# Kernel tuning notes

Hardware: AMD Instinct MI355X
Metric: run time of the kernel (lower is better)

The kernel has to match this reference:

```python
import jax, jax.numpy as jnp
import numpy as np

D = 768
EPS = 1e-5

def _layernorm(x, g, b):
    mu = jnp.mean(x, axis=-1, keepdims=True)
    var = jnp.mean(jnp.square(x - mu), axis=-1, keepdims=True)
    return (x - mu) * jax.lax.rsqrt(var + EPS) * g + b

def setup_inputs() -> dict:
    key = jax.random.key(0)
    ks = jax.random.split(key, 12)
    s = 1.0 / np.sqrt(D)
    x = jax.random.normal(ks[0], (8, 2048, D), dtype=jnp.float32)
    Wq = jax.random.uniform(ks[1], (D, D), jnp.float32, -s, s)
    bq = jax.random.uniform(ks[2], (D,), jnp.float32, -s, s)
    Wk = jax.random.uniform(ks[3], (D, D), jnp.float32, -s, s)
    bk = jax.random.uniform(ks[4], (D,), jnp.float32, -s, s)
    Wv = jax.random.uniform(ks[5], (D, D), jnp.float32, -s, s)
    bv = jax.random.uniform(ks[6], (D,), jnp.float32, -s, s)
    W1 = jax.random.uniform(ks[7], (D, D), jnp.float32, -s, s)
    b1 = jax.random.uniform(ks[8], (D,), jnp.float32, -s, s)
    W2 = jax.random.uniform(ks[9], (D, D), jnp.float32, -s, s)
    b2 = jax.random.uniform(ks[10], (D,), jnp.float32, -s, s)
    g_n1 = jnp.ones((D,), jnp.float32); be_n1 = jnp.zeros((D,), jnp.float32)
    g_n2 = jnp.ones((D,), jnp.float32); be_n2 = jnp.zeros((D,), jnp.float32)
    return {"x": x, "Wq": Wq, "bq": bq, "Wk": Wk, "bk": bk, "Wv": Wv, "bv": bv,
            "W1": W1, "b1": b1, "W2": W2, "b2": b2,
            "g_n1": g_n1, "be_n1": be_n1, "g_n2": g_n2, "be_n2": be_n2}

def reference(x, Wq, bq, Wk, bk, Wv, bv, W1, b1, W2, b2, g_n1, be_n1, g_n2, be_n2):
    # pre-norm single-head self-attention (scores materialized as in source)
    h = _layernorm(x, g_n1, be_n1)
    q = h @ Wq.T + bq  # [B,S,D]
    k = h @ Wk.T + bk
    v = h @ Wv.T + bv
    scores = jnp.einsum('bsd,btd->bst', q, k) / jnp.sqrt(jnp.float32(D))
    attn = jax.nn.softmax(scores, axis=-1)
    x = jnp.einsum('bst,btd->bsd', attn, v) + x
    # MLP: two Linear(d,d) each followed by exact GELU (matches source MLP)
    h = _layernorm(x, g_n2, be_n2)
    h = jax.nn.gelu(h @ W1.T + b1, approximate=False)
    h = jax.nn.gelu(h @ W2.T + b2, approximate=False)
    return h + x
```

## Files before the change

kernel.cpp:

```cpp
#include <hip/hip_runtime.h>
#include <cstdint>
#include <cstddef>

#define D_MODEL 768
#define NBATCH 8
#define SEQLEN 2048
#define NROWS (NBATCH*SEQLEN)

typedef __attribute__((ext_vector_type(4))) float  f32x4;
typedef __attribute__((ext_vector_type(8))) __bf16 bf16x8;
typedef __attribute__((ext_vector_type(4))) __bf16 bf16x4;
typedef __attribute__((ext_vector_type(8))) _Float16 f16x8;

#define MFMA16(a,b,c) __builtin_amdgcn_mfma_f32_16x16x32_bf16(a,b,c,0,0,0)
#define SCALE 0.03608439182435161f
#define AS1 __attribute__((address_space(1)))
#define AS3 __attribute__((address_space(3)))

static constexpr size_t SZ_ACT = (size_t)NROWS * D_MODEL * 2;
static constexpr size_t OFF_Q    = 0;
static constexpr size_t OFF_K    = OFF_Q + SZ_ACT;
static constexpr size_t OFF_VT   = OFF_K + SZ_ACT;
static constexpr size_t OFF_X2   = OFF_VT + SZ_ACT;
static constexpr size_t OFF_W    = OFF_X2 + (size_t)NROWS*D_MODEL*4;
static constexpr size_t OFF_POOL = OFF_W + (size_t)5*589824*2;

__device__ __forceinline__ float gelu_exact(float x) {
  return 0.5f * x * (1.0f + erff(x * 0.70710678118654752f));
}

__device__ __forceinline__ int xcd_remap(int p, int chunk) {
  return (p & 7) * chunk + (p >> 3);
}

__global__ __launch_bounds__(256) void k_cvt5(
    const float* __restrict__ s0, const float* __restrict__ s1,
    const float* __restrict__ s2, const float* __restrict__ s3,
    const float* __restrict__ s4, __bf16* __restrict__ dst)
{
  const int wsel = blockIdx.y;
  const float* s = wsel==0 ? s0 : wsel==1 ? s1 : wsel==2 ? s2 : wsel==3 ? s3 : s4;
  const size_t i = ((size_t)blockIdx.x*256 + threadIdx.x)*4;
  float4 v = *(const float4*)(s + i);
  bf16x4 o;
  o[0] = (__bf16)v.x; o[1] = (__bf16)v.y; o[2] = (__bf16)v.z; o[3] = (__bf16)v.w;
  *(bf16x4*)(dst + (size_t)wsel*589824 + i) = o;
}

__global__ __launch_bounds__(256) void k_layernorm(
    const float* __restrict__ x, const float* __restrict__ g,
    const float* __restrict__ be, __bf16* __restrict__ out)
{
  const int row  = blockIdx.x*4 + (threadIdx.x>>6);
  const int lane = threadIdx.x & 63;
  const float4* xr = (const float4*)(x + (size_t)row*D_MODEL);
  float4 v[3];
  float s = 0.f, ss = 0.f;
#pragma unroll
  for (int j=0;j<3;j++){
    v[j] = xr[lane + 64*j];
    s  += v[j].x + v[j].y + v[j].z + v[j].w;
    ss += v[j].x*v[j].x + v[j].y*v[j].y + v[j].z*v[j].z + v[j].w*v[j].w;
  }
#pragma unroll
  for (int d=1; d<64; d<<=1){ s += __shfl_xor(s,d); ss += __shfl_xor(ss,d); }
  const float mu   = s  * (1.f/768.f);
  const float var  = ss * (1.f/768.f) - mu*mu;
  const float rstd = rsqrtf(var + 1e-5f);
  __bf16* orow = out + (size_t)row*D_MODEL;
#pragma unroll
  for (int j=0;j<3;j++){
    const int c0 = (lane + 64*j)*4;
    bf16x4 o;
    o[0] = (__bf16)((v[j].x - mu)*rstd*g[c0+0] + be[c0+0]);
    o[1] = (__bf16)((v[j].y - mu)*rstd*g[c0+1] + be[c0+1]);
    o[2] = (__bf16)((v[j].z - mu)*rstd*g[c0+2] + be[c0+2]);
    o[3] = (__bf16)((v[j].w - mu)*rstd*g[c0+3] + be[c0+3]);
    *(bf16x4*)(orow + c0) = o;
  }
}

__global__ __launch_bounds__(256) void k_softmax(_Float16* __restrict__ S)
{
  const int row  = blockIdx.x*4 + (threadIdx.x>>6);
  const int lane = threadIdx.x & 63;
  _Float16* sr = S + (size_t)row*SEQLEN + lane*32;
  f16x8 v[4];
#pragma unroll
  for (int j=0;j<4;j++) v[j] = *(const f16x8*)(sr + j*8);
  float f[32];
  float mx = -1e30f;
#pragma unroll
  for (int j=0;j<4;j++)
#pragma unroll
    for (int e=0;e<8;e++){ f[j*8+e] = (float)v[j][e]; mx = fmaxf(mx, f[j*8+e]); }
#pragma unroll
  for (int d=1; d<64; d<<=1) mx = fmaxf(mx, __shfl_xor(mx, d));
  float sum = 0.f;
#pragma unroll
  for (int i=0;i<32;i++){ f[i] = __expf(f[i]-mx); sum += f[i]; }
#pragma unroll
  for (int d=1; d<64; d<<=1) sum += __shfl_xor(sum, d);
  const float inv = 1.f/sum;
  __bf16* pr = (__bf16*)(S + (size_t)row*SEQLEN) + lane*32;
#pragma unroll
  for (int j=0;j<4;j++){
    bf16x8 o;
#pragma unroll
    for (int e=0;e<8;e++) o[e] = (__bf16)(f[j*8+e]*inv);
    *(bf16x8*)(pr + j*8) = o;
  }
}

template<int NT>
__device__ __forceinline__ void gemm_core_rp(
    const __bf16* __restrict__ Asrc, const int ldA,
    const __bf16* __restrict__ Bsrc, const int ldB,
    f32x4 (&acc)[4][4])
{
  __shared__ __bf16 As[2*4096];
  __shared__ __bf16 Bs[2*4096];
  const int tid = threadIdx.x, w = tid>>6, lane = tid&63;
  const int wr = w>>1, wc = w&1, l16 = lane&15, l4 = lane>>4;

  const int rql   = l16>>1;
  const int rslot = (((l16&1)<<2) + l4) ^ rql;
  const int roff  = rql*64 + rslot*8;

  const int su  = (lane&7) ^ (lane>>3);
  const int ss_ = (su>>2)&1;
  const int sg_ = su&3;
  const int srw = 2*(lane>>3) + ss_;
  const int sco = sg_*8;

#pragma unroll
  for (int mi=0;mi<4;mi++)
#pragma unroll
    for (int ni=0;ni<4;ni++)
      acc[mi][ni] = (f32x4){0.f,0.f,0.f,0.f};

#define STGRP(T_) { \
    const int kb_ = (T_)*32; \
    const int sb_ = ((T_)&1)*4096; \
    _Pragma("unroll") \
    for (int i_=0;i_<2;i_++){ \
      const int ii_ = w + i_*4; \
      const int rg_ = ii_*16 + srw; \
      __builtin_amdgcn_global_load_lds((const AS1 void*)(Asrc + (size_t)rg_*ldA + kb_ + sco), (AS3 void*)(As + sb_ + ii_*512), 16, 0, 0); \
      __builtin_amdgcn_global_load_lds((const AS1 void*)(Bsrc + (size_t)rg_*ldB + kb_ + sco), (AS3 void*)(Bs + sb_ + ii_*512), 16, 0, 0); \
    } }

  STGRP(0) STGRP(1)

  for (int t=0; t<NT; ++t){
    if (t+1 < NT) asm volatile("s_waitcnt vmcnt(4)" ::: "memory");
    else          asm volatile("s_waitcnt vmcnt(0)" ::: "memory");
    __builtin_amdgcn_s_barrier();
    const int sb = (t&1)*4096;
    bf16x8 af[4], bq[4];
#pragma unroll
    for (int mi=0;mi<4;mi++)
      af[mi] = *(const bf16x8*)(As + sb + (wr*32 + mi*8)*64 + roff);
#pragma unroll
    for (int ni=0;ni<4;ni++)
      bq[ni] = *(const bf16x8*)(Bs + sb + (wc*32 + ni*8)*64 + roff);
    asm volatile("s_waitcnt lgkmcnt(0)" ::: "memory");
    __builtin_amdgcn_sched_barrier(0);
    __builtin_amdgcn_s_barrier();
    if (t+2 < NT) STGRP(t+2)
    __builtin_amdgcn_s_setprio(1);
#pragma unroll
    for (int mi=0;mi<4;mi++)
#pragma unroll
      for (int ni=0;ni<4;ni++)
        acc[mi][ni] = MFMA16(af[mi], bq[ni], acc[mi][ni]);
    __builtin_amdgcn_s_setprio(0);
  }
#undef STGRP
}

__global__ __launch_bounds__(256) void k_qkv(
    const __bf16* __restrict__ A, const __bf16* __restrict__ W,
    const float* __restrict__ bq, const float* __restrict__ bk, const float* __restrict__ bv,
    __bf16* __restrict__ Cq, __bf16* __restrict__ Ck, __bf16* __restrict__ vT)
{
  const int L = xcd_remap(blockIdx.x, 288);
  const int bm = L/18, bn = L%18;
  f32x4 acc[4][4];
  gemm_core_rp<24>(A + (size_t)bm*128*D_MODEL, D_MODEL, W + (size_t)bn*128*D_MODEL, D_MODEL, acc);
  const int tid = threadIdx.x, w=tid>>6, lane=tid&63;
  const int wr=w>>1, wc=w&1, l16=lane&15, l4=lane>>4;
  const int seg = bn/6;
  const int colb = (bn%6)*128 + wc*64;
  const int row0 = bm*128 + wr*64;
  if (seg < 2){
    const float* bias = seg==0 ? bq : bk;
    __bf16* C = seg==0 ? Cq : Ck;
#pragma unroll
    for (int ni=0;ni<4;ni++){
      const int col = colb + ni*16 + l16;
      const float bb = bias[col];
#pragma unroll
      for (int mi=0;mi<4;mi++)
#pragma unroll
        for (int r=0;r<4;r++){
          const int row = row0 + mi*16 + l4*4 + r;
          float v = acc[mi][ni][r] + bb;
          if (seg==0) v *= SCALE;
          C[(size_t)row*D_MODEL + col] = (__bf16)v;
        }
    }
  } else {
    const int b = row0 >> 11;
    const int trow0 = row0 & 2047;
    __bf16* vtb = vT + (size_t)b*D_MODEL*SEQLEN;
#pragma unroll
    for (int ni=0;ni<4;ni++){
      const int col = colb + ni*16 + l16;
      const float bb = bv[col];
#pragma unroll
      for (int mi=0;mi<4;mi++){
        bf16x4 o;
#pragma unroll
        for (int r=0;r<4;r++) o[r] = (__bf16)(acc[mi][ni][r] + bb);
        *(bf16x4*)(vtb + (size_t)col*SEQLEN + trow0 + mi*16 + l4*4) = o;
      }
    }
  }
}

__global__ __launch_bounds__(256) void k_s(
    const __bf16* __restrict__ Q, const __bf16* __restrict__ K, _Float16* __restrict__ S,
    int chunk)
{
  const int L = xcd_remap(blockIdx.x, chunk);
  const int batch = L>>8, r = L&255;
  const int bm = r>>4, bn = r&15;
  const size_t bo = (size_t)batch * SEQLEN * D_MODEL;
  f32x4 acc[4][4];
  gemm_core_rp<24>(Q + bo + (size_t)bm*128*D_MODEL, D_MODEL, K + bo + (size_t)bn*128*D_MODEL, D_MODEL, acc);
  const int tid = threadIdx.x, w=tid>>6, lane=tid&63;
  const int wr=w>>1, wc=w&1, l16=lane&15, l4=lane>>4;
  _Float16* Sb = S + (size_t)batch*SEQLEN*SEQLEN;
  const int row0 = bm*128 + wr*64, col0 = bn*128 + wc*64;
#pragma unroll
  for (int ni=0;ni<4;ni++){
    const int col = col0 + ni*16 + l16;
#pragma unroll
    for (int mi=0;mi<4;mi++)
#pragma unroll
      for (int r2=0;r2<4;r2++)
        Sb[(size_t)(row0 + mi*16 + l4*4 + r2)*SEQLEN + col] = (_Float16)acc[mi][ni][r2];
  }
}

__global__ __launch_bounds__(256) void k_pv(
    const __bf16* __restrict__ P, const __bf16* __restrict__ VT,
    const float* __restrict__ x, float* __restrict__ x2, int bbase, int chunk)
{
  const int L = xcd_remap(blockIdx.x, chunk);
  const int by = L/96, r = L%96;
  const int bm = r/6, bn = r%6;
  const int bidx = bbase + by;
  f32x4 acc[4][4];
  gemm_core_rp<64>(P + (size_t)by*SEQLEN*SEQLEN + (size_t)bm*128*SEQLEN, SEQLEN,
                   VT + (size_t)bidx*D_MODEL*SEQLEN + (size_t)bn*128*SEQLEN, SEQLEN, acc);
  const int tid = threadIdx.x, w=tid>>6, lane=tid&63;
  const int wr=w>>1, wc=w&1, l16=lane&15, l4=lane>>4;
  const size_t row0 = (size_t)bidx*SEQLEN + bm*128 + wr*64;
  const int col0 = bn*128 + wc*64;
#pragma unroll
  for (int ni=0;ni<4;ni++){
    const int col = col0 + ni*16 + l16;
#pragma unroll
    for (int mi=0;mi<4;mi++)
#pragma unroll
      for (int r2=0;r2<4;r2++){
        const size_t row = row0 + mi*16 + l4*4 + r2;
        x2[row*D_MODEL + col] = acc[mi][ni][r2] + x[row*D_MODEL + col];
      }
  }
}

template<int RES>
__global__ __launch_bounds__(256) void k_mlp(
    const __bf16* __restrict__ A, const __bf16* __restrict__ W,
    const float* __restrict__ bias, const float* __restrict__ resid, void* __restrict__ out)
{
  const int L = xcd_remap(blockIdx.x, 96);
  const int bm = L/6, bn = L%6;
  f32x4 acc[4][4];
  gemm_core_rp<24>(A + (size_t)bm*128*D_MODEL, D_MODEL, W + (size_t)bn*128*D_MODEL, D_MODEL, acc);
  const int tid = threadIdx.x, w=tid>>6, lane=tid&63;
  const int wr=w>>1, wc=w&1, l16=lane&15, l4=lane>>4;
  const int row0 = bm*128 + wr*64, col0 = bn*128 + wc*64;
#pragma unroll
  for (int ni=0;ni<4;ni++){
    const int col = col0 + ni*16 + l16;
    const float bb = bias[col];
#pragma unroll
    for (int mi=0;mi<4;mi++)
#pragma unroll
      for (int r=0;r<4;r++){
        const int row = row0 + mi*16 + l4*4 + r;
        float v = gelu_exact(acc[mi][ni][r] + bb);
        if (RES) ((float*)out)[(size_t)row*D_MODEL + col] = v + resid[(size_t)row*D_MODEL + col];
        else     ((__bf16*)out)[(size_t)row*D_MODEL + col] = (__bf16)v;
      }
  }
}

extern "C" void kernel_launch(void* const* d_in, const int* in_sizes, int n_in,
                              void* d_out, int out_size, void* d_ws, size_t ws_size,
                              hipStream_t stream)
{
  const float* x   = (const float*)d_in[0];
  const float* Wq  = (const float*)d_in[1];
  const float* bq  = (const float*)d_in[2];
  const float* Wk  = (const float*)d_in[3];
  const float* bk  = (const float*)d_in[4];
  const float* Wv  = (const float*)d_in[5];
  const float* bv  = (const float*)d_in[6];
  const float* W1  = (const float*)d_in[7];
  const float* b1  = (const float*)d_in[8];
  const float* W2  = (const float*)d_in[9];
  const float* b2  = (const float*)d_in[10];
  const float* g1  = (const float*)d_in[11];
  const float* be1 = (const float*)d_in[12];
  const float* g2  = (const float*)d_in[13];
  const float* be2 = (const float*)d_in[14];
  (void)in_sizes; (void)n_in; (void)out_size;

  char* ws = (char*)d_ws;
  __bf16*   qb  = (__bf16*)(ws + OFF_Q);
  __bf16*   kb  = (__bf16*)(ws + OFF_K);
  __bf16*   vT  = (__bf16*)(ws + OFF_VT);
  float*    x2  = (float*)(ws + OFF_X2);
  __bf16*   wbf = (__bf16*)(ws + OFF_W);
  __bf16*   h1  = (__bf16*)(ws + OFF_POOL);
  _Float16* Sp  = (_Float16*)(ws + OFF_POOL);
  __bf16*   h2  = h1;
  __bf16*   h3  = qb;

  const bool big = ws_size >= OFF_POOL + (size_t)NBATCH*SEQLEN*SEQLEN*2;

  k_cvt5<<<dim3(576,5,1),256,0,stream>>>(Wq,Wk,Wv,W1,W2,wbf);
  k_layernorm<<<dim3(4096),256,0,stream>>>(x, g1, be1, h1);
  k_qkv<<<dim3(2304),256,0,stream>>>(h1, wbf, bq, bk, bv, qb, kb, vT);

  if (big){
    k_s<<<dim3(2048),256,0,stream>>>(qb, kb, Sp, 256);
    k_softmax<<<dim3(4096),256,0,stream>>>(Sp);
    k_pv<<<dim3(768),256,0,stream>>>((const __bf16*)Sp, vT, x, x2, 0, 96);
  } else {
    for (int c=0;c<2;c++){
      const size_t qoff = (size_t)c*4*SEQLEN*D_MODEL;
      k_s<<<dim3(1024),256,0,stream>>>(qb + qoff, kb + qoff, Sp, 128);
      k_softmax<<<dim3(2048),256,0,stream>>>(Sp);
      k_pv<<<dim3(384),256,0,stream>>>((const __bf16*)Sp, vT, x, x2, c*4, 48);
    }
  }

  k_layernorm<<<dim3(4096),256,0,stream>>>(x2, g2, be2, h2);
  k_mlp<0><<<dim3(768),256,0,stream>>>(h2, wbf + (size_t)3*589824, b1, nullptr, h3);
  k_mlp<1><<<dim3(768),256,0,stream>>>(h3, wbf + (size_t)4*589824, b2, x2, d_out);
}
```

Before: 384.7 us.

## Replace double-buffered GEMM core with single-buffer BK=64 swizzled tile loop

The shared GEMM core moves from a two-stage double-buffered pipeline with a K tile of 32 to a single-buffer loop with a K tile of 64. It now loads, waits for all loads, computes two MFMA substeps and then synchronises, so it runs half as many iterations and barriers per tile. It also uses a simpler XOR swizzle to avoid LDS bank conflicts. The cost is that global loads no longer overlap with MFMA work inside a block, so latency hiding depends on other resident blocks. LDS per block is unchanged.

```diff
diff --git a/kernel.cpp b/kernel.cpp
--- a/kernel.cpp
+++ b/kernel.cpp
@@ -113,25 +113,18 @@
 }
 
 template<int NT>
-__device__ __forceinline__ void gemm_core_rp(
+__device__ __forceinline__ void gemm_core_sb(
     const __bf16* __restrict__ Asrc, const int ldA,
     const __bf16* __restrict__ Bsrc, const int ldB,
     f32x4 (&acc)[4][4])
 {
-  __shared__ __bf16 As[2*4096];
-  __shared__ __bf16 Bs[2*4096];
+  __shared__ __bf16 As[128*64];
+  __shared__ __bf16 Bs[128*64];
   const int tid = threadIdx.x, w = tid>>6, lane = tid&63;
   const int wr = w>>1, wc = w&1, l16 = lane&15, l4 = lane>>4;
-
-  const int rql   = l16>>1;
-  const int rslot = (((l16&1)<<2) + l4) ^ rql;
-  const int roff  = rql*64 + rslot*8;
-
-  const int su  = (lane&7) ^ (lane>>3);
-  const int ss_ = (su>>2)&1;
-  const int sg_ = su&3;
-  const int srw = 2*(lane>>3) + ss_;
-  const int sco = sg_*8;
+  const int sro = lane>>3;
+  const int sgr = ((lane&7) ^ (lane>>3))*8;
+  const int rxr = l16 & 7;
 
 #pragma unroll
   for (int mi=0;mi<4;mi++)
@@ -139,44 +132,40 @@
     for (int ni=0;ni<4;ni++)
       acc[mi][ni] = (f32x4){0.f,0.f,0.f,0.f};
 
-#define STGRP(T_) { \
-    const int kb_ = (T_)*32; \
-    const int sb_ = ((T_)&1)*4096; \
-    _Pragma("unroll") \
-    for (int i_=0;i_<2;i_++){ \
-      const int ii_ = w + i_*4; \
-      const int rg_ = ii_*16 + srw; \
-      __builtin_amdgcn_global_load_lds((const AS1 void*)(Asrc + (size_t)rg_*ldA + kb_ + sco), (AS3 void*)(As + sb_ + ii_*512), 16, 0, 0); \
-      __builtin_amdgcn_global_load_lds((const AS1 void*)(Bsrc + (size_t)rg_*ldB + kb_ + sco), (AS3 void*)(Bs + sb_ + ii_*512), 16, 0, 0); \
-    } }
-
-  STGRP(0) STGRP(1)
-
   for (int t=0; t<NT; ++t){
-    if (t+1 < NT) asm volatile("s_waitcnt vmcnt(4)" ::: "memory");
-    else          asm volatile("s_waitcnt vmcnt(0)" ::: "memory");
+#pragma unroll
+    for (int i=0;i<4;i++){
+      const int strip = w*4 + i;
+      const int rg = strip*8 + sro;
+      __builtin_amdgcn_global_load_lds(
+        (const AS1 void*)(Asrc + (size_t)rg*ldA + t*64 + sgr),
+        (AS3 void*)(As + strip*512), 16, 0, 0);
+      __builtin_amdgcn_global_load_lds(
+        (const AS1 void*)(Bsrc + (size_t)rg*ldB + t*64 + sgr),
+        (AS3 void*)(Bs + strip*512), 16, 0, 0);
+    }
+    asm volatile("s_waitcnt vmcnt(0)" ::: "memory");
     __builtin_amdgcn_s_barrier();
-    const int sb = (t&1)*4096;
-    bf16x8 af[4], bq[4];
-#pragma unroll
-    for (int mi=0;mi<4;mi++)
-      af[mi] = *(const bf16x8*)(As + sb + (wr*32 + mi*8)*64 + roff);
-#pragma unroll
-    for (int ni=0;ni<4;ni++)
-      bq[ni] = *(const bf16x8*)(Bs + sb + (wc*32 + ni*8)*64 + roff);
-    asm volatile("s_waitcnt lgkmcnt(0)" ::: "memory");
-    __builtin_amdgcn_sched_barrier(0);
+
+#pragma unroll
+    for (int kk=0;kk<2;kk++){
+      bf16x8 af[4], bq[4];
+#pragma unroll
+      for (int mi=0;mi<4;mi++)
+        af[mi] = *(const bf16x8*)(As + (wr*64 + mi*16 + l16)*64 + (((kk*4 + l4) ^ rxr))*8);
+#pragma unroll
+      for (int ni=0;ni<4;ni++)
+        bq[ni] = *(const bf16x8*)(Bs + (wc*64 + ni*16 + l16)*64 + (((kk*4 + l4) ^ rxr))*8);
+      __builtin_amdgcn_s_setprio(1);
+#pragma unroll
+      for (int mi=0;mi<4;mi++)
+#pragma unroll
+        for (int ni=0;ni<4;ni++)
+          acc[mi][ni] = MFMA16(af[mi], bq[ni], acc[mi][ni]);
+      __builtin_amdgcn_s_setprio(0);
+    }
     __builtin_amdgcn_s_barrier();
-    if (t+2 < NT) STGRP(t+2)
-    __builtin_amdgcn_s_setprio(1);
-#pragma unroll
-    for (int mi=0;mi<4;mi++)
-#pragma unroll
-      for (int ni=0;ni<4;ni++)
-        acc[mi][ni] = MFMA16(af[mi], bq[ni], acc[mi][ni]);
-    __builtin_amdgcn_s_setprio(0);
-  }
-#undef STGRP
+  }
 }
 
 __global__ __launch_bounds__(256) void k_qkv(
@@ -187,7 +176,7 @@
   const int L = xcd_remap(blockIdx.x, 288);
   const int bm = L/18, bn = L%18;
   f32x4 acc[4][4];
-  gemm_core_rp<24>(A + (size_t)bm*128*D_MODEL, D_MODEL, W + (size_t)bn*128*D_MODEL, D_MODEL, acc);
+  gemm_core_sb<12>(A + (size_t)bm*128*D_MODEL, D_MODEL, W + (size_t)bn*128*D_MODEL, D_MODEL, acc);
   const int tid = threadIdx.x, w=tid>>6, lane=tid&63;
   const int wr=w>>1, wc=w&1, l16=lane&15, l4=lane>>4;
   const int seg = bn/6;
@@ -238,7 +227,7 @@
   const int bm = r>>4, bn = r&15;
   const size_t bo = (size_t)batch * SEQLEN * D_MODEL;
   f32x4 acc[4][4];
-  gemm_core_rp<24>(Q + bo + (size_t)bm*128*D_MODEL, D_MODEL, K + bo + (size_t)bn*128*D_MODEL, D_MODEL, acc);
+  gemm_core_sb<12>(Q + bo + (size_t)bm*128*D_MODEL, D_MODEL, K + bo + (size_t)bn*128*D_MODEL, D_MODEL, acc);
   const int tid = threadIdx.x, w=tid>>6, lane=tid&63;
   const int wr=w>>1, wc=w&1, l16=lane&15, l4=lane>>4;
   _Float16* Sb = S + (size_t)batch*SEQLEN*SEQLEN;
@@ -263,7 +252,7 @@
   const int bm = r/6, bn = r%6;
   const int bidx = bbase + by;
   f32x4 acc[4][4];
-  gemm_core_rp<64>(P + (size_t)by*SEQLEN*SEQLEN + (size_t)bm*128*SEQLEN, SEQLEN,
+  gemm_core_sb<32>(P + (size_t)by*SEQLEN*SEQLEN + (size_t)bm*128*SEQLEN, SEQLEN,
                    VT + (size_t)bidx*D_MODEL*SEQLEN + (size_t)bn*128*SEQLEN, SEQLEN, acc);
   const int tid = threadIdx.x, w=tid>>6, lane=tid&63;
   const int wr=w>>1, wc=w&1, l16=lane&15, l4=lane>>4;
@@ -290,7 +279,7 @@
   const int L = xcd_remap(blockIdx.x, 96);
   const int bm = L/6, bn = L%6;
   f32x4 acc[4][4];
-  gemm_core_rp<24>(A + (size_t)bm*128*D_MODEL, D_MODEL, W + (size_t)bn*128*D_MODEL, D_MODEL, acc);
+  gemm_core_sb<12>(A + (size_t)bm*128*D_MODEL, D_MODEL, W + (size_t)bn*128*D_MODEL, D_MODEL, acc);
   const int tid = threadIdx.x, w=tid>>6, lane=tid&63;
   const int wr=w>>1, wc=w&1, l16=lane&15, l4=lane>>4;
   const int row0 = bm*128 + wr*64, col0 = bn*128 + wc*64;
```

Result: slower. 400.5 us (+4.1%).

## Fuse softmax into score GEMM epilogue and deferred normalization in PV

Applied to the files above, without the earlier changes.

Removes the standalone softmax kernel. The score GEMM epilogue now applies exp directly and writes bf16 probabilities. It also writes per-tile row partial sums to a small buffer, reduced across wavefronts through shared memory. The PV kernel sums those partials and scales its accumulator by the reciprocal row sum before the residual add. This avoids a full read and write pass over the large score matrix, but drops the max subtraction, so it relies on the scaled scores staying small enough that exp does not overflow.

```diff
diff --git a/kernel.cpp b/kernel.cpp
--- a/kernel.cpp
+++ b/kernel.cpp
@@ -10,7 +10,6 @@
 typedef __attribute__((ext_vector_type(4))) float  f32x4;
 typedef __attribute__((ext_vector_type(8))) __bf16 bf16x8;
 typedef __attribute__((ext_vector_type(4))) __bf16 bf16x4;
-typedef __attribute__((ext_vector_type(8))) _Float16 f16x8;
 
 #define MFMA16(a,b,c) __builtin_amdgcn_mfma_f32_16x16x32_bf16(a,b,c,0,0,0)
 #define SCALE 0.03608439182435161f
@@ -80,46 +79,13 @@
   }
 }
 
-__global__ __launch_bounds__(256) void k_softmax(_Float16* __restrict__ S)
-{
-  const int row  = blockIdx.x*4 + (threadIdx.x>>6);
-  const int lane = threadIdx.x & 63;
-  _Float16* sr = S + (size_t)row*SEQLEN + lane*32;
-  f16x8 v[4];
-#pragma unroll
-  for (int j=0;j<4;j++) v[j] = *(const f16x8*)(sr + j*8);
-  float f[32];
-  float mx = -1e30f;
-#pragma unroll
-  for (int j=0;j<4;j++)
-#pragma unroll
-    for (int e=0;e<8;e++){ f[j*8+e] = (float)v[j][e]; mx = fmaxf(mx, f[j*8+e]); }
-#pragma unroll
-  for (int d=1; d<64; d<<=1) mx = fmaxf(mx, __shfl_xor(mx, d));
-  float sum = 0.f;
-#pragma unroll
-  for (int i=0;i<32;i++){ f[i] = __expf(f[i]-mx); sum += f[i]; }
-#pragma unroll
-  for (int d=1; d<64; d<<=1) sum += __shfl_xor(sum, d);
-  const float inv = 1.f/sum;
-  __bf16* pr = (__bf16*)(S + (size_t)row*SEQLEN) + lane*32;
-#pragma unroll
-  for (int j=0;j<4;j++){
-    bf16x8 o;
-#pragma unroll
-    for (int e=0;e<8;e++) o[e] = (__bf16)(f[j*8+e]*inv);
-    *(bf16x8*)(pr + j*8) = o;
-  }
-}
-
 template<int NT>
 __device__ __forceinline__ void gemm_core_rp(
+    __bf16* __restrict__ As, __bf16* __restrict__ Bs,
     const __bf16* __restrict__ Asrc, const int ldA,
     const __bf16* __restrict__ Bsrc, const int ldB,
     f32x4 (&acc)[4][4])
 {
-  __shared__ __bf16 As[2*4096];
-  __shared__ __bf16 Bs[2*4096];
   const int tid = threadIdx.x, w = tid>>6, lane = tid&63;
   const int wr = w>>1, wc = w&1, l16 = lane&15, l4 = lane>>4;
 
@@ -184,10 +150,12 @@
     const float* __restrict__ bq, const float* __restrict__ bk, const float* __restrict__ bv,
     __bf16* __restrict__ Cq, __bf16* __restrict__ Ck, __bf16* __restrict__ vT)
 {
+  __shared__ __bf16 As[2*4096];
+  __shared__ __bf16 Bs[2*4096];
   const int L = xcd_remap(blockIdx.x, 288);
   const int bm = L/18, bn = L%18;
   f32x4 acc[4][4];
-  gemm_core_rp<24>(A + (size_t)bm*128*D_MODEL, D_MODEL, W + (size_t)bn*128*D_MODEL, D_MODEL, acc);
+  gemm_core_rp<24>(As, Bs, A + (size_t)bm*128*D_MODEL, D_MODEL, W + (size_t)bn*128*D_MODEL, D_MODEL, acc);
   const int tid = threadIdx.x, w=tid>>6, lane=tid&63;
   const int wr=w>>1, wc=w&1, l16=lane&15, l4=lane>>4;
   const int seg = bn/6;
@@ -230,43 +198,88 @@
 }
 
 __global__ __launch_bounds__(256) void k_s(
-    const __bf16* __restrict__ Q, const __bf16* __restrict__ K, _Float16* __restrict__ S,
-    int chunk)
-{
+    const __bf16* __restrict__ Q, const __bf16* __restrict__ K,
+    __bf16* __restrict__ S, float* __restrict__ Spart, int chunk)
+{
+  __shared__ __bf16 As[2*4096];
+  __shared__ __bf16 Bs[2*4096];
   const int L = xcd_remap(blockIdx.x, chunk);
   const int batch = L>>8, r = L&255;
   const int bm = r>>4, bn = r&15;
   const size_t bo = (size_t)batch * SEQLEN * D_MODEL;
   f32x4 acc[4][4];
-  gemm_core_rp<24>(Q + bo + (size_t)bm*128*D_MODEL, D_MODEL, K + bo + (size_t)bn*128*D_MODEL, D_MODEL, acc);
+  gemm_core_rp<24>(As, Bs, Q + bo + (size_t)bm*128*D_MODEL, D_MODEL, K + bo + (size_t)bn*128*D_MODEL, D_MODEL, acc);
   const int tid = threadIdx.x, w=tid>>6, lane=tid&63;
   const int wr=w>>1, wc=w&1, l16=lane&15, l4=lane>>4;
-  _Float16* Sb = S + (size_t)batch*SEQLEN*SEQLEN;
+  __bf16* Sb = S + (size_t)batch*SEQLEN*SEQLEN;
   const int row0 = bm*128 + wr*64, col0 = bn*128 + wc*64;
+  float rp[4][4] = {};
 #pragma unroll
   for (int ni=0;ni<4;ni++){
     const int col = col0 + ni*16 + l16;
 #pragma unroll
     for (int mi=0;mi<4;mi++)
 #pragma unroll
-      for (int r2=0;r2<4;r2++)
-        Sb[(size_t)(row0 + mi*16 + l4*4 + r2)*SEQLEN + col] = (_Float16)acc[mi][ni][r2];
-  }
+      for (int r2=0;r2<4;r2++){
+        const float e = __expf(acc[mi][ni][r2]);
+        const __bf16 eb = (__bf16)e;
+        Sb[(size_t)(row0 + mi*16 + l4*4 + r2)*SEQLEN + col] = eb;
+        rp[mi][r2] += (float)eb;
+      }
+  }
+#pragma unroll
+  for (int mi=0;mi<4;mi++)
+#pragma unroll
+    for (int r2=0;r2<4;r2++){
+#pragma unroll
+      for (int d=1; d<16; d<<=1) rp[mi][r2] += __shfl_xor(rp[mi][r2], d);
+    }
+  __syncthreads();
+  float* part = (float*)Bs;
+  if (wc==0 && l16==0){
+#pragma unroll
+    for (int mi=0;mi<4;mi++)
+#pragma unroll
+      for (int r2=0;r2<4;r2++) part[wr*64 + mi*16 + l4*4 + r2] = rp[mi][r2];
+  }
+  __syncthreads();
+  if (wc==1 && l16==0){
+#pragma unroll
+    for (int mi=0;mi<4;mi++)
+#pragma unroll
+      for (int r2=0;r2<4;r2++) part[wr*64 + mi*16 + l4*4 + r2] += rp[mi][r2];
+  }
+  __syncthreads();
+  if (tid < 128)
+    Spart[((size_t)batch*SEQLEN + bm*128 + tid)*16 + bn] = part[tid];
 }
 
 __global__ __launch_bounds__(256) void k_pv(
-    const __bf16* __restrict__ P, const __bf16* __restrict__ VT,
+    const __bf16* __restrict__ P, const float* __restrict__ Spart,
+    const __bf16* __restrict__ VT,
     const float* __restrict__ x, float* __restrict__ x2, int bbase, int chunk)
 {
+  __shared__ __bf16 As[2*4096];
+  __shared__ __bf16 Bs[2*4096];
   const int L = xcd_remap(blockIdx.x, chunk);
   const int by = L/96, r = L%96;
   const int bm = r/6, bn = r%6;
   const int bidx = bbase + by;
   f32x4 acc[4][4];
-  gemm_core_rp<64>(P + (size_t)by*SEQLEN*SEQLEN + (size_t)bm*128*SEQLEN, SEQLEN,
+  gemm_core_rp<64>(As, Bs, P + (size_t)by*SEQLEN*SEQLEN + (size_t)bm*128*SEQLEN, SEQLEN,
                    VT + (size_t)bidx*D_MODEL*SEQLEN + (size_t)bn*128*SEQLEN, SEQLEN, acc);
   const int tid = threadIdx.x, w=tid>>6, lane=tid&63;
   const int wr=w>>1, wc=w&1, l16=lane&15, l4=lane>>4;
+  __syncthreads();
+  float* rs = (float*)Bs;
+  if (tid < 128){
+    const float* sp = Spart + ((size_t)by*SEQLEN + bm*128 + tid)*16;
+    float s = 0.f;
+#pragma unroll
+    for (int b=0;b<16;b++) s += sp[b];
+    rs[tid] = 1.0f / s;
+  }
+  __syncthreads();
   const size_t row0 = (size_t)bidx*SEQLEN + bm*128 + wr*64;
   const int col0 = bn*128 + wc*64;
 #pragma unroll
@@ -277,7 +290,8 @@
 #pragma unroll
       for (int r2=0;r2<4;r2++){
         const size_t row = row0 + mi*16 + l4*4 + r2;
-        x2[row*D_MODEL + col] = acc[mi][ni][r2] + x[row*D_MODEL + col];
+        const float inv = rs[wr*64 + mi*16 + l4*4 + r2];
+        x2[row*D_MODEL + col] = acc[mi][ni][r2]*inv + x[row*D_MODEL + col];
       }
   }
 }
@@ -287,10 +301,12 @@
     const __bf16* __restrict__ A, const __bf16* __restrict__ W,
     const float* __restrict__ bias, const float* __restrict__ resid, void* __restrict__ out)
 {
+  __shared__ __bf16 As[2*4096];
+  __shared__ __bf16 Bs[2*4096];
   const int L = xcd_remap(blockIdx.x, 96);
   const int bm = L/6, bn = L%6;
   f32x4 acc[4][4];
-  gemm_core_rp<24>(A + (size_t)bm*128*D_MODEL, D_MODEL, W + (size_t)bn*128*D_MODEL, D_MODEL, acc);
+  gemm_core_rp<24>(As, Bs, A + (size_t)bm*128*D_MODEL, D_MODEL, W + (size_t)bn*128*D_MODEL, D_MODEL, acc);
   const int tid = threadIdx.x, w=tid>>6, lane=tid&63;
   const int wr=w>>1, wc=w&1, l16=lane&15, l4=lane>>4;
   const int row0 = bm*128 + wr*64, col0 = bn*128 + wc*64;
@@ -338,26 +354,28 @@
   float*    x2  = (float*)(ws + OFF_X2);
   __bf16*   wbf = (__bf16*)(ws + OFF_W);
   __bf16*   h1  = (__bf16*)(ws + OFF_POOL);
-  _Float16* Sp  = (_Float16*)(ws + OFF_POOL);
+  __bf16*   Sp  = (__bf16*)(ws + OFF_POOL);
   __bf16*   h2  = h1;
   __bf16*   h3  = qb;
 
-  const bool big = ws_size >= OFF_POOL + (size_t)NBATCH*SEQLEN*SEQLEN*2;
+  const size_t szS8 = (size_t)NBATCH*SEQLEN*SEQLEN*2;
+  const size_t szP8 = (size_t)NBATCH*SEQLEN*16*4;
+  const bool big = ws_size >= OFF_POOL + szS8 + szP8;
 
   k_cvt5<<<dim3(576,5,1),256,0,stream>>>(Wq,Wk,Wv,W1,W2,wbf);
   k_layernorm<<<dim3(4096),256,0,stream>>>(x, g1, be1, h1);
   k_qkv<<<dim3(2304),256,0,stream>>>(h1, wbf, bq, bk, bv, qb, kb, vT);
 
   if (big){
-    k_s<<<dim3(2048),256,0,stream>>>(qb, kb, Sp, 256);
-    k_softmax<<<dim3(4096),256,0,stream>>>(Sp);
-    k_pv<<<dim3(768),256,0,stream>>>((const __bf16*)Sp, vT, x, x2, 0, 96);
+    float* Spart = (float*)(ws + OFF_POOL + szS8);
+    k_s<<<dim3(2048),256,0,stream>>>(qb, kb, Sp, Spart, 256);
+    k_pv<<<dim3(768),256,0,stream>>>(Sp, Spart, vT, x, x2, 0, 96);
   } else {
+    float* Spart = (float*)(ws + OFF_POOL + (size_t)4*SEQLEN*SEQLEN*2);
     for (int c=0;c<2;c++){
       const size_t qoff = (size_t)c*4*SEQLEN*D_MODEL;
-      k_s<<<dim3(1024),256,0,stream>>>(qb + qoff, kb + qoff, Sp, 128);
-      k_softmax<<<dim3(2048),256,0,stream>>>(Sp);
-      k_pv<<<dim3(384),256,0,stream>>>((const __bf16*)Sp, vT, x, x2, c*4, 48);
+      k_s<<<dim3(1024),256,0,stream>>>(qb + qoff, kb + qoff, Sp, Spart, 128);
+      k_pv<<<dim3(384),256,0,stream>>>(Sp, Spart, vT, x, x2, c*4, 48);
     }
   }
 
```

Measured after the change: 399.0 us. 1.04x slower.
